# Optimization experiments

Measured on AMD Instinct MI355X. Metric: run time of the kernel, lower is better.

The kernel has to match this reference:

```python
import jax, jax.numpy as jnp
from jax import lax
import numpy as np

GAMMA = 0.5
LENS = 0.3
B_J0 = 0.1
# eval-mode BN with running_mean=0, running_var=1, weight=0.1, bias=0 -> pure scale
BN_SCALE = 0.1 / np.sqrt(1.0 + 1e-5)


def _gaussian(x, mu, sigma):
    return jnp.exp(-(x - mu) ** 2 / (2.0 * sigma ** 2)) / np.sqrt(2.0 * np.pi) / sigma


@jax.custom_vjp
def act_fun_adp(x):
    return (x > 0).astype(x.dtype)


def _act_fwd(x):
    return act_fun_adp(x), x


def _act_bwd(x, g):
    scale, hight = 6.0, 0.15
    temp = (_gaussian(x, 0.0, LENS) * (1.0 + hight)
            - _gaussian(x, LENS, scale * LENS) * hight
            - _gaussian(x, -LENS, scale * LENS) * hight)
    return (g * temp * GAMMA,)


act_fun_adp.defvjp(_act_fwd, _act_bwd)


def _lin(x, w, b):
    return x @ w.T + b


def _mem_update_adp(inp, mem, spk, tau_adp, tau_m, b):
    b = tau_adp * b + (1.0 - tau_adp) * spk
    B = B_J0 + 1.8 * b
    mem = mem + (-mem + inp) * tau_m
    spk = act_fun_adp(mem - B)
    mem = (1.0 - spk) * mem
    return mem, spk, b


def _snn(inputs, h, p):
    (w1x, b1x, w1r, b1r, w1m, b1m, w1a, b1a,
     w2x, b2x, w2r, b2r, w2m, b2m, w2a, b2a,
     w3x, b3x, w3m, b3m) = p

    def step(h, x):
        mem1, spk1, bb1, mem2, spk2, bb2, mem3 = h
        dense1 = BN_SCALE * _lin(x, w1x, b1x) + BN_SCALE * _lin(spk1, w1r, b1r)
        tauM1 = jax.nn.sigmoid(_lin(jnp.concatenate([dense1, mem1], -1), w1m, b1m))
        tauA1 = jax.nn.sigmoid(_lin(jnp.concatenate([dense1, bb1], -1), w1a, b1a))
        nmem1, nspk1, nbb1 = _mem_update_adp(dense1, mem1, spk1, tauA1, tauM1, bb1)
        # dropout in eval mode = identity; layer2_r uses PREVIOUS spk1 (h[1]) as in source
        dense2 = BN_SCALE * _lin(nspk1, w2x, b2x) + BN_SCALE * _lin(spk1, w2r, b2r)
        tauM2 = jax.nn.sigmoid(_lin(jnp.concatenate([dense2, mem2], -1), w2m, b2m))
        tauA2 = jax.nn.sigmoid(_lin(jnp.concatenate([dense2, bb2], -1), w2a, b2a))
        nmem2, nspk2, nbb2 = _mem_update_adp(dense2, mem2, spk2, tauA2, tauM2, bb2)
        dense3 = BN_SCALE * _lin(nspk2, w3x, b3x)
        tauM3 = jax.nn.sigmoid(_lin(jnp.concatenate([dense3, mem3], -1), w3m, b3m))
        nmem3 = (1.0 - tauM3) * mem3 + dense3 * tauM3
        out = jax.nn.log_softmax(nmem3, axis=1)
        return (nmem1, nspk1, nbb1, nmem2, nspk2, nbb2, nmem3), out

    xs = jnp.swapaxes(inputs, 0, 1)  # [T, B, Din]
    hT, outs = lax.scan(step, h, xs)
    return outs, hT  # outs: [T, B, O]


def setup_inputs() -> dict:
    key = jax.random.key(0)
    B, T, DIN, H, O = 128, 100, 700, 1024, 20
    ks = jax.random.split(key, 16)
    d = {
        'inputs': jax.random.normal(ks[0], (B, T, DIN), jnp.float32),
        'h0': jnp.zeros((B, H)), 'h1': jnp.zeros((B, H)), 'h2': jnp.zeros((B, H)),
        'h3': jnp.zeros((B, H)), 'h4': jnp.zeros((B, H)), 'h5': jnp.zeros((B, H)),
        'h6': jnp.zeros((B, O)),
        'w1x': jax.random.normal(ks[1], (H, DIN)) * 0.03,
        'b1x': jnp.zeros((H,)),
        'w1r': jax.random.normal(ks[2], (H, H)) * 0.03,
        'b1r': jnp.zeros((H,)),
        'w1m': jax.random.normal(ks[3], (H, 2 * H)) * 0.02,
        'b1m': jnp.zeros((H,)),
        'w1a': jax.random.normal(ks[4], (H, 2 * H)) * 0.02,
        'b1a': jnp.zeros((H,)),
        'w2x': jax.random.normal(ks[5], (H, H)) * 0.03,
        'b2x': jnp.zeros((H,)),
        'w2r': jax.random.normal(ks[6], (H, H)) * 0.03,
        'b2r': jnp.zeros((H,)),
        'w2m': jax.random.normal(ks[7], (H, 2 * H)) * 0.02,
        'b2m': jnp.zeros((H,)),
        'w2a': jax.random.normal(ks[8], (H, 2 * H)) * 0.02,
        'b2a': jnp.zeros((H,)),
        'w3x': jax.random.normal(ks[9], (O, H)) * 0.03,
        'b3x': jnp.zeros((O,)),
        'w3m': jax.random.normal(ks[10], (O, 2 * O)) * 0.02,
        'b3m': jnp.zeros((O,)),
    }
    return d


def reference(inputs, h0, h1, h2, h3, h4, h5, h6,
              w1x, b1x, w1r, b1r, w1m, b1m, w1a, b1a,
              w2x, b2x, w2r, b2r, w2m, b2m, w2a, b2a,
              w3x, b3x, w3m, b3m):
    h = (h0, h1, h2, h3, h4, h5, h6)
    p = (w1x, b1x, w1r, b1r, w1m, b1m, w1a, b1a,
         w2x, b2x, w2r, b2r, w2m, b2m, w2a, b2a,
         w3x, b3x, w3m, b3m)
    outs, hT = _snn(inputs, h, p)
    return (outs,) + hT
```

## Files before the change

kernel.cpp:

```cpp
#include <hip/hip_runtime.h>
#include <cmath>


namespace {

constexpr int BB = 128, TT = 100, DIN = 700, HH = 1024, OO = 20;
constexpr int BH = BB * HH;
constexpr int XP = 704;
constexpr float SBN = 0.09999950000374996f;

typedef __attribute__((ext_vector_type(8))) __bf16 bf16x8;
typedef __attribute__((ext_vector_type(4))) float f32x4;

__device__ __forceinline__ float sigm(float x) { return 1.f / (1.f + expf(-x)); }

__device__ __forceinline__ unsigned short f2bf(float x) {
  union { float f; unsigned u; } a; a.f = x;
  unsigned u = a.u; u += 0x7fffu + ((u >> 16) & 1u);
  return (unsigned short)(u >> 16);
}
__device__ __forceinline__ float bf2f(unsigned short h) {
  union { unsigned u; float f; } a; a.u = ((unsigned)h) << 16; return a.f;
}


struct MSeg {
  const unsigned short* Ah; const unsigned short* Al;
  const unsigned short* Wh; const unsigned short* Wl;
  float* P;
  int ldk, KS, nsplit, nblkn, mbs, ldp;
  size_t planesz;
};
struct MArgs { MSeg s[8]; int bstart[9]; int nseg; };

__global__ __launch_bounds__(256)
void mfma_seg(MArgs ma) {
  int bid = blockIdx.x, si = 0;
  while (si + 1 < ma.nseg && bid >= ma.bstart[si + 1]) si++;
  MSeg sg = ma.s[si]; bid -= ma.bstart[si];
  const int per_m = sg.nblkn * sg.nsplit;
  const int mb = bid / per_m;
  const int rr = bid - mb * per_m;
  const int nb = rr / sg.nsplit, sp = rr - nb * sg.nsplit;
  const int n0 = nb * 64;
  const int m0 = mb * 128;
  const int kbeg = sp * sg.KS, kend = kbeg + sg.KS;
  const int lane = threadIdx.x & 63, wave = threadIdx.x >> 6;
  const int wm = (wave >> 1) * 64, wn = (wave & 1) * 32;
  const int quad = lane >> 4, r16 = lane & 15;
  const int ldk = sg.ldk;
  const int nkb = ldk >> 5;
  const bool three = (sg.Al != nullptr);
  const unsigned short* ah = sg.Ah + (size_t)(m0 + wm + r16) * ldk + quad * 8;
  const unsigned short* al = three ? sg.Al + (size_t)(m0 + wm + r16) * ldk + quad * 8 : ah;
  const size_t tb = (size_t)((n0 + wn) >> 4) * nkb * 512 + (size_t)lane * 8;
  const unsigned short* wh = sg.Wh + tb;
  const unsigned short* wl = sg.Wl + tb;

  f32x4 acc[4][2];
#pragma unroll
  for (int i = 0; i < 4; i++)
#pragma unroll
    for (int j = 0; j < 2; j++) acc[i][j] = (f32x4){0.f, 0.f, 0.f, 0.f};

  auto loadf = [&](int k, bf16x8* Ab, bf16x8* ALb, bf16x8* Bb, bf16x8* BLb) {
    const int kb = k >> 5;
#pragma unroll
    for (int mt = 0; mt < 4; mt++)
      Ab[mt] = *(const bf16x8*)(ah + (size_t)mt * 16 * ldk + k);
#pragma unroll
    for (int nt = 0; nt < 2; nt++) {
      Bb[nt] = *(const bf16x8*)(wh + ((size_t)nt * nkb + kb) * 512);
      BLb[nt] = *(const bf16x8*)(wl + ((size_t)nt * nkb + kb) * 512);
    }
    if (three) {
#pragma unroll
      for (int mt = 0; mt < 4; mt++)
        ALb[mt] = *(const bf16x8*)(al + (size_t)mt * 16 * ldk + k);
    }
  };
  auto domfma = [&](bf16x8* Ab, bf16x8* ALb, bf16x8* Bb, bf16x8* BLb) {
#pragma unroll
    for (int mt = 0; mt < 4; mt++)
#pragma unroll
      for (int nt = 0; nt < 2; nt++) {
        acc[mt][nt] = __builtin_amdgcn_mfma_f32_16x16x32_bf16(Ab[mt], Bb[nt], acc[mt][nt], 0, 0, 0);
        acc[mt][nt] = __builtin_amdgcn_mfma_f32_16x16x32_bf16(Ab[mt], BLb[nt], acc[mt][nt], 0, 0, 0);
        if (three)
          acc[mt][nt] = __builtin_amdgcn_mfma_f32_16x16x32_bf16(ALb[mt], Bb[nt], acc[mt][nt], 0, 0, 0);
      }
  };

  bf16x8 A0[4], L0[4], B0[2], C0[2];
  bf16x8 A1[4], L1[4], B1[2], C1[2];
  int k = kbeg;
  loadf(k, A0, L0, B0, C0);
  while (true) {
    int k1 = k + 32;
    bool more1 = k1 < kend;
    if (more1) loadf(k1, A1, L1, B1, C1);
    domfma(A0, L0, B0, C0);
    if (!more1) break;
    int k2 = k1 + 32;
    bool more2 = k2 < kend;
    if (more2) loadf(k2, A0, L0, B0, C0);
    domfma(A1, L1, B1, C1);
    if (!more2) break;
    k = k2;
  }

  const int outl = n0 >> 10;
  const int col0 = (n0 & 1023) + wn;
  float* P = sg.P + (size_t)(outl * sg.nsplit + sp) * sg.planesz;
#pragma unroll
  for (int mt = 0; mt < 4; mt++)
#pragma unroll
    for (int nt = 0; nt < 2; nt++)
#pragma unroll
      for (int r = 0; r < 4; r++)
        P[(size_t)(m0 + wm + mt * 16 + quad * 4 + r) * sg.ldp + col0 + nt * 16 + r16] = acc[mt][nt][r];
}

struct CJob { const float* src; int ldsrc, rows, cols, rrows, mode; unsigned short* dh; unsigned short* dl; int lddst; float scale; };
struct CArgs { CJob j[16]; int bstart[17]; int njob; };

__global__ __launch_bounds__(256)
void cvt_pack(CArgs ca) {
  int bid = blockIdx.x, ji = 0;
  while (ji + 1 < ca.njob && bid >= ca.bstart[ji + 1]) ji++;
  CJob j = ca.j[ji]; bid -= ca.bstart[ji];
  size_t total = (size_t)j.rows * j.lddst;
  size_t base = ((size_t)bid * 256 + threadIdx.x) * 4;
  const int nkb = j.lddst >> 5;
#pragma unroll
  for (int e = 0; e < 4; e++) {
    size_t i = base + e;
    if (i >= total) break;
    int r, c;
    if (j.mode == 2) {
      r = (int)(i / j.lddst); c = (int)(i - (size_t)r * j.lddst);
    } else {
      size_t tile = i >> 9;
      int within = (int)(i & 511);
      int lane = within >> 3, jj = within & 7;
      int r16 = lane & 15, quad = lane >> 4;
      int ntile = (int)(tile / nkb), kb = (int)(tile - (size_t)ntile * nkb);
      r = ntile * 16 + r16;
      c = kb * 32 + quad * 8 + jj;
    }
    float v = 0.f;
    if (c < j.cols && r < j.rrows)
      v = j.scale * (j.mode == 1 ? j.src[(size_t)c * j.ldsrc + r]
                                 : j.src[(size_t)r * j.ldsrc + c]);
    unsigned short hh = f2bf(v);
    j.dh[i] = hh;
    j.dl[i] = f2bf(v - bf2f(hh));
  }
}

__global__ __launch_bounds__(256)
void init_state(const float* h0, const float* h1, const float* h2, const float* h3,
                const float* h4, const float* h5, const float* h6, const float* inputs,
                float* mem1, float* spk1, float* bb1, float* mem2, float* spk2, float* bb2,
                float* mem3, unsigned short* spk1bf,
                unsigned short* m1h, unsigned short* m1l, unsigned short* b1h, unsigned short* b1l,
                unsigned short* m2h, unsigned short* m2l, unsigned short* b2h, unsigned short* b2l,
                unsigned short* xh0, unsigned short* xl0) {
  int idx = blockIdx.x * 256 + threadIdx.x;
  if (idx < BH) {
    float v;
    v = h0[idx]; mem1[idx] = v; { unsigned short h = f2bf(v); m1h[idx] = h; m1l[idx] = f2bf(v - bf2f(h)); }
    v = h1[idx]; spk1[idx] = v; spk1bf[idx] = f2bf(v);
    v = h2[idx]; bb1[idx] = v;  { unsigned short h = f2bf(v); b1h[idx] = h; b1l[idx] = f2bf(v - bf2f(h)); }
    v = h3[idx]; mem2[idx] = v; { unsigned short h = f2bf(v); m2h[idx] = h; m2l[idx] = f2bf(v - bf2f(h)); }
    spk2[idx] = h4[idx];
    v = h5[idx]; bb2[idx] = v;  { unsigned short h = f2bf(v); b2h[idx] = h; b2l[idx] = f2bf(v - bf2f(h)); }
  }
  if (idx < BB * OO) mem3[idx] = h6[idx];
  if (idx < BB * XP) {
    int b = idx / XP, c = idx - b * XP;
    float v = (c < DIN) ? inputs[(size_t)b * TT * DIN + c] : 0.f;
    unsigned short hh = f2bf(v);
    xh0[idx] = hh; xl0[idx] = f2bf(v - bf2f(hh));
  }
}

__global__ __launch_bounds__(256)
void ew1m(const float* Pbuf, const float* b1x, const float* b1r,
          const float* cb1m, const float* cb1a,
          float* mem1, float* spk1, float* bb1, unsigned short* spk1bf,
          unsigned short* m1h, unsigned short* m1l, unsigned short* b1h_, unsigned short* b1l_) {
  int idx = blockIdx.x * 256 + threadIdx.x;
  int n = idx & (HH - 1);
  constexpr int D1S[6]   = {0, 1, 6, 7, 8, 9};
  constexpr int T1MS[10] = {2, 3, 10, 11, 12, 13, 30, 31, 32, 33};
  constexpr int T1AS[10] = {4, 5, 14, 15, 16, 17, 34, 35, 36, 37};
  float d1 = SBN * (b1x[n] + b1r[n]);
#pragma unroll
  for (int i = 0; i < 6; i++) d1 += Pbuf[(size_t)D1S[i] * BH + idx];
  float pm = cb1m[n];
#pragma unroll
  for (int i = 0; i < 10; i++) pm += Pbuf[(size_t)T1MS[i] * BH + idx];
  float pa = cb1a[n];
#pragma unroll
  for (int i = 0; i < 10; i++) pa += Pbuf[(size_t)T1AS[i] * BH + idx];
  float tM = sigm(pm), tA = sigm(pa);
  float spo = spk1[idx], bo = bb1[idx], mo = mem1[idx];
  float nb = tA * bo + (1.f - tA) * spo;
  float Bth = 0.1f + 1.8f * nb;
  float nm = mo + (d1 - mo) * tM;
  float sp = (nm - Bth) > 0.f ? 1.f : 0.f;
  nm = (1.f - sp) * nm;
  mem1[idx] = nm; spk1[idx] = sp; bb1[idx] = nb;
  spk1bf[idx] = f2bf(sp);
  { unsigned short h = f2bf(nm); m1h[idx] = h; m1l[idx] = f2bf(nm - bf2f(h)); }
  { unsigned short h = f2bf(nb); b1h_[idx] = h; b1l_[idx] = f2bf(nb - bf2f(h)); }
}

__global__ __launch_bounds__(1024)
void ew2l3m(const float* Pbuf, const float* b2x, const float* b2r,
            const float* cb2m, const float* cb2a,
            float* mem2, float* spk2, float* bb2, float* mem3,
            unsigned short* m2h, unsigned short* m2l, unsigned short* b2h_, unsigned short* b2l_,
            const float* w3x, const float* b3x, const float* w3m, const float* b3m,
            float* outs, const float* inputs, unsigned short* xh_next, unsigned short* xl_next,
            int t) {
  int b = blockIdx.x;
  int n = threadIdx.x;
  size_t idx = (size_t)b * HH + n;
  constexpr int D2S[8]   = {18, 19, 20, 21, 46, 47, 48, 49};
  constexpr int T2MS[12] = {22, 23, 24, 25, 38, 39, 40, 41, 50, 51, 52, 53};
  constexpr int T2AS[12] = {26, 27, 28, 29, 42, 43, 44, 45, 54, 55, 56, 57};
  float d2 = SBN * (b2x[n] + b2r[n]);
#pragma unroll
  for (int i = 0; i < 8; i++) d2 += Pbuf[(size_t)D2S[i] * BH + idx];
  float pm = cb2m[n];
#pragma unroll
  for (int i = 0; i < 12; i++) pm += Pbuf[(size_t)T2MS[i] * BH + idx];
  float pa = cb2a[n];
#pragma unroll
  for (int i = 0; i < 12; i++) pa += Pbuf[(size_t)T2AS[i] * BH + idx];
  float tM = sigm(pm), tA = sigm(pa);
  float spo = spk2[idx], bo = bb2[idx], mo = mem2[idx];
  float nb = tA * bo + (1.f - tA) * spo;
  float Bth = 0.1f + 1.8f * nb;
  float nm = mo + (d2 - mo) * tM;
  float sp = (nm - Bth) > 0.f ? 1.f : 0.f;
  nm = (1.f - sp) * nm;
  mem2[idx] = nm; spk2[idx] = sp; bb2[idx] = nb;
  { unsigned short h = f2bf(nm); m2h[idx] = h; m2l[idx] = f2bf(nm - bf2f(h)); }
  { unsigned short h = f2bf(nb); b2h_[idx] = h; b2l_[idx] = f2bf(nb - bf2f(h)); }

  if (t + 1 < TT && n < XP) {
    float v = (n < DIN) ? inputs[((size_t)b * TT + (t + 1)) * DIN + n] : 0.f;
    unsigned short hh = f2bf(v);
    xh_next[b * XP + n] = hh;
    xl_next[b * XP + n] = f2bf(v - bf2f(hh));
  }

  __shared__ float smsp[HH];
  __shared__ float d3s[OO];
  __shared__ float nm3s[OO];
  smsp[n] = sp;
  __syncthreads();

  int wv = n >> 6, ln = n & 63;
  for (int o = wv; o < OO; o += 16) {
    float s = 0.f;
    for (int j = ln; j < HH; j += 64) s += smsp[j] * w3x[(size_t)o * HH + j];
    for (int off = 32; off > 0; off >>= 1) s += __shfl_down(s, off, 64);
    if (ln == 0) d3s[o] = SBN * (s + b3x[o]);
  }
  __syncthreads();

  if (n < OO) {
    float acc = b3m[n];
#pragma unroll
    for (int k = 0; k < OO; k++) acc += d3s[k] * w3m[n * 40 + k];
#pragma unroll
    for (int k = 0; k < OO; k++) acc += mem3[b * OO + k] * w3m[n * 40 + 20 + k];
    float tau = sigm(acc);
    nm3s[n] = (1.f - tau) * mem3[b * OO + n] + d3s[n] * tau;
  }
  __syncthreads();

  if (n < OO) {
    float mx = -1e30f;
#pragma unroll
    for (int k = 0; k < OO; k++) mx = fmaxf(mx, nm3s[k]);
    float se = 0.f;
#pragma unroll
    for (int k = 0; k < OO; k++) se += expf(nm3s[k] - mx);
    float lse = mx + logf(se);
    outs[((size_t)t * BB + b) * OO + n] = nm3s[n] - lse;
    mem3[b * OO + n] = nm3s[n];
  }
}


struct Seg {
  const float* A; const float* W; float* P;
  int lda, ldw, ldp, K, KS, nsplit, mblks, nblks, nbound, xmap, xoff;
  float scale;
};
constexpr int MAXSEG = 13;
struct SegArgs { Seg s[MAXSEG]; int bstart[MAXSEG + 1]; int nseg; };

__global__ __launch_bounds__(256)
void seg_gemm(SegArgs sa) {
  int bid = blockIdx.x;
  int si = 0;
  while (si + 1 < sa.nseg && bid >= sa.bstart[si + 1]) si++;
  const Seg sg = sa.s[si];
  bid -= sa.bstart[si];
  const int per_m = sg.nblks * sg.nsplit;
  const int mb = bid / per_m;
  const int rr = bid - mb * per_m;
  const int nb = rr / sg.nsplit;
  const int sp = rr - nb * sg.nsplit;
  const int m0 = mb * 128, n0 = nb * 32;
  const int kbeg = sp * sg.KS;
  const int kend = min(sg.K, kbeg + sg.KS);

  __shared__ float As[32][132];
  __shared__ float Ws[32][36];

  const int t = threadIdx.x;
  const int cg = t & 7;
  const int rg = t >> 3;

  float acc[4][4];
#pragma unroll
  for (int i = 0; i < 4; i++)
#pragma unroll
    for (int j = 0; j < 4; j++) acc[i][j] = 0.f;

  for (int k0 = kbeg; k0 < kend; k0 += 32) {
#pragma unroll
    for (int i = 0; i < 4; i++) {
      int fl = t + i * 256;
      int row = fl >> 3, kq = fl & 7;
      int kg = k0 + kq * 4;
      float4 v = make_float4(0.f, 0.f, 0.f, 0.f);
      if (kg < kend) {
        const float* src = sg.xmap
            ? sg.A + ((size_t)(m0 + row) * TT + sg.xoff) * DIN + kg
            : sg.A + (size_t)(m0 + row) * sg.lda + kg;
        v = *(const float4*)src;
      }
      As[kq * 4 + 0][row] = v.x;
      As[kq * 4 + 1][row] = v.y;
      As[kq * 4 + 2][row] = v.z;
      As[kq * 4 + 3][row] = v.w;
    }
    {
      int n = t >> 3, kq = t & 7;
      int kg = k0 + kq * 4;
      float4 v = make_float4(0.f, 0.f, 0.f, 0.f);
      if (kg < kend && (n0 + n) < sg.nbound)
        v = *(const float4*)(sg.W + (size_t)(n0 + n) * sg.ldw + kg);
      Ws[kq * 4 + 0][n] = v.x;
      Ws[kq * 4 + 1][n] = v.y;
      Ws[kq * 4 + 2][n] = v.z;
      Ws[kq * 4 + 3][n] = v.w;
    }
    __syncthreads();
#pragma unroll
    for (int kk = 0; kk < 32; kk++) {
      float4 av = *(const float4*)&As[kk][rg * 4];
      float4 wv = *(const float4*)&Ws[kk][cg * 4];
      acc[0][0] += av.x * wv.x; acc[0][1] += av.x * wv.y; acc[0][2] += av.x * wv.z; acc[0][3] += av.x * wv.w;
      acc[1][0] += av.y * wv.x; acc[1][1] += av.y * wv.y; acc[1][2] += av.y * wv.z; acc[1][3] += av.y * wv.w;
      acc[2][0] += av.z * wv.x; acc[2][1] += av.z * wv.y; acc[2][2] += av.z * wv.z; acc[2][3] += av.z * wv.w;
      acc[3][0] += av.w * wv.x; acc[3][1] += av.w * wv.y; acc[3][2] += av.w * wv.z; acc[3][3] += av.w * wv.w;
    }
    __syncthreads();
  }
  float* P = sg.P + ((size_t)sp * sg.mblks * 128 + m0) * sg.ldp;
#pragma unroll
  for (int i = 0; i < 4; i++) {
    float4 v = make_float4(sg.scale * acc[i][0], sg.scale * acc[i][1],
                           sg.scale * acc[i][2], sg.scale * acc[i][3]);
    *(float4*)&P[(size_t)(rg * 4 + i) * sg.ldp + n0 + cg * 4] = v;
  }
}

struct TJob { const float* src; float* dst; int rows, cols, ntc; };
struct TArgs { TJob j[4]; int tstart[5]; };

__global__ __launch_bounds__(256)
void transpose4(TArgs ta) {
  int bid = blockIdx.x;
  int ji = 0;
  while (ji + 1 < 4 && bid >= ta.tstart[ji + 1]) ji++;
  TJob j = ta.j[ji];
  bid -= ta.tstart[ji];
  int tr = bid / j.ntc, tc = bid - tr * j.ntc;
  int r0 = tr * 32, c0 = tc * 32;
  __shared__ float tile[32][33];
  int tx = threadIdx.x & 31, ty = threadIdx.x >> 5;
#pragma unroll
  for (int p = 0; p < 4; p++) {
    int r = r0 + ty + p * 8, c = c0 + tx;
    if (r < j.rows && c < j.cols) tile[ty + p * 8][tx] = j.src[(size_t)r * j.cols + c];
  }
  __syncthreads();
#pragma unroll
  for (int p = 0; p < 4; p++) {
    int c = c0 + ty + p * 8, r = r0 + tx;
    if (c < j.cols && r < j.rows) j.dst[(size_t)c * j.rows + r] = tile[tx][ty + p * 8];
// ... 408 lines not shown
  float* mem1 = ws + off; off += BH;
  float* spk1 = ws + off; off += BH;
  float* bb1  = ws + off; off += BH;
  float* mem2 = ws + off; off += BH;
  float* spk2 = ws + off; off += BH;
  float* bb2  = ws + off; off += BH;
  float* mem3 = ws + off; off += BB * OO;
  float* cb1m = ws + off; off += HH;
  float* cb1a = ws + off; off += HH;
  float* cb2m = ws + off; off += HH;
  float* cb2a = ws + off; off += HH;
  float* w1rT = ws + off; off += (size_t)HH * HH;
  float* w2rT = ws + off; off += (size_t)HH * HH;
  float* w2xT = ws + off; off += (size_t)HH * HH;
  float* w1xT = ws + off; off += (size_t)DIN * HH;
  float* G1mT  = ws + off; off += (size_t)HH * HH;
  float* G1aT  = ws + off; off += (size_t)HH * HH;
  float* H1MT  = ws + off; off += (size_t)HH * 704;
  float* H1AT  = ws + off; off += (size_t)HH * 704;
  float* G2rmT = ws + off; off += (size_t)HH * HH;
  float* G2raT = ws + off; off += (size_t)HH * HH;
  float* G2xmT = ws + off; off += (size_t)HH * HH;
  float* G2xaT = ws + off; off += (size_t)HH * HH;
  float* Pbuf  = ws + off; off += (size_t)32 * BH;
  if (ws_size < off * sizeof(float)) {
    launch_tier3(d_in, d_out, d_ws, ws_size, stream);
    return;
  }

  hipMemcpyAsync(mem1, h[0], (size_t)BH * 4, hipMemcpyDeviceToDevice, stream);
  hipMemcpyAsync(spk1, h[1], (size_t)BH * 4, hipMemcpyDeviceToDevice, stream);
  hipMemcpyAsync(bb1,  h[2], (size_t)BH * 4, hipMemcpyDeviceToDevice, stream);
  hipMemcpyAsync(mem2, h[3], (size_t)BH * 4, hipMemcpyDeviceToDevice, stream);
  hipMemcpyAsync(spk2, h[4], (size_t)BH * 4, hipMemcpyDeviceToDevice, stream);
  hipMemcpyAsync(bb2,  h[5], (size_t)BH * 4, hipMemcpyDeviceToDevice, stream);
  hipMemcpyAsync(mem3, h[6], (size_t)BB * OO * 4, hipMemcpyDeviceToDevice, stream);

  {
    TArgs ta{};
    ta.j[0] = TJob{w1r, w1rT, HH, HH, 32};
    ta.j[1] = TJob{w2r, w2rT, HH, HH, 32};
    ta.j[2] = TJob{w2x, w2xT, HH, HH, 32};
    ta.j[3] = TJob{w1x, w1xT, HH, DIN, 22};
    ta.tstart[0] = 0; ta.tstart[1] = 1024; ta.tstart[2] = 2048;
    ta.tstart[3] = 3072; ta.tstart[4] = 3072 + 32 * 22;
    transpose4<<<ta.tstart[4], 256, 0, stream>>>(ta);
  }
  bias_prep<<<1024, 256, 0, stream>>>(b1x, b1r, b2x, b2r, w1m, b1m, w1a, b1a,
                                      w2m, b2m, w2a, b2a, cb1m, cb1a, cb2m, cb2a);
  {
    SegArgs sa{};
    int nb = 0, c = 0;
    auto add = [&](const float* A, int lda, const float* W, int ldw, int nbound,
                   float* P, int ldp, int nblks) {
      sa.s[c] = Seg{A, W, P, lda, ldw, ldp, HH, HH, 1, 8, nblks, nbound, 0, 0, 1.0f};
      sa.bstart[c] = nb; nb += 8 * nblks; c++;
    };
    add(w1m, 2048, w1rT, 1024, 1024, G1mT, 1024, 32);
    add(w1a, 2048, w1rT, 1024, 1024, G1aT, 1024, 32);
    add(w1m, 2048, w1xT, 1024, DIN, H1MT, 704, 22);
    add(w1a, 2048, w1xT, 1024, DIN, H1AT, 704, 22);
    add(w2m, 2048, w2rT, 1024, 1024, G2rmT, 1024, 32);
    add(w2a, 2048, w2rT, 1024, 1024, G2raT, 1024, 32);
    add(w2m, 2048, w2xT, 1024, 1024, G2xmT, 1024, 32);
    add(w2a, 2048, w2xT, 1024, 1024, G2xaT, 1024, 32);
    sa.bstart[c] = nb; sa.nseg = c;
    seg_gemm<<<nb, 256, 0, stream>>>(sa);
  }

  for (int t = 0; t < TT; ++t) {
    {
      SegArgs sa{};
      int nb = 0, c = 0;
      auto add = [&](const float* A, int lda, int xmap, const float* W, int ldw,
                     int K, int KS, int slot, float scale) {
        sa.s[c] = Seg{A, W, Pbuf + (size_t)slot * BH, lda, ldw, 1024, K, KS, 2, 1, 32,
                      1024, xmap, t, scale};
        sa.bstart[c] = nb; nb += 64; c++;
      };
      add(inputs, 0, 1, w1x, DIN, DIN, 352, 0, SBN);
      add(spk1, 1024, 0, w1r, 1024, 1024, 512, 2, SBN);
      add(inputs, 0, 1, H1MT, 704, DIN, 352, 4, SBN);
      add(spk1, 1024, 0, G1mT, 1024, 1024, 512, 6, SBN);
      add(mem1, 1024, 0, w1m + 1024, 2048, 1024, 512, 8, 1.0f);
      add(inputs, 0, 1, H1AT, 704, DIN, 352, 10, SBN);
      add(spk1, 1024, 0, G1aT, 1024, 1024, 512, 12, SBN);
      add(bb1, 1024, 0, w1a + 1024, 2048, 1024, 512, 14, 1.0f);
      add(spk1, 1024, 0, w2r, 1024, 1024, 512, 16, SBN);
      add(spk1, 1024, 0, G2rmT, 1024, 1024, 512, 18, SBN);
      add(mem2, 1024, 0, w2m + 1024, 2048, 1024, 512, 20, 1.0f);
      add(spk1, 1024, 0, G2raT, 1024, 1024, 512, 22, SBN);
      add(bb2, 1024, 0, w2a + 1024, 2048, 1024, 512, 24, 1.0f);
      sa.bstart[c] = nb; sa.nseg = c;
      seg_gemm<<<nb, 256, 0, stream>>>(sa);
    }
    ew1<<<BH / 256, 256, 0, stream>>>(Pbuf, b1x, b1r, cb1m, cb1a, mem1, spk1, bb1);
    {
      SegArgs sa{};
      int nb = 0, c = 0;
      auto add = [&](const float* W, int slot) {
        sa.s[c] = Seg{spk1, W, Pbuf + (size_t)slot * BH, 1024, 1024, 1024, 1024, 512,
                      2, 1, 32, 1024, 0, 0, SBN};
        sa.bstart[c] = nb; nb += 64; c++;
      };
      add(w2x, 26);
      add(G2xmT, 28);
      add(G2xaT, 30);
      sa.bstart[c] = nb; sa.nseg = c;
      seg_gemm<<<nb, 256, 0, stream>>>(sa);
    }
    ew2_layer3<<<BB, 1024, 0, stream>>>(Pbuf, b2x, b2r, cb2m, cb2a, mem2, spk2, bb2,
                                        mem3, w3x, b3x, w3m, b3m, (float*)d_out, t);
  }

  float* out = (float*)d_out;
  size_t o = (size_t)TT * BB * OO;
  hipMemcpyAsync(out + o, mem1, (size_t)BH * 4, hipMemcpyDeviceToDevice, stream); o += BH;
  hipMemcpyAsync(out + o, spk1, (size_t)BH * 4, hipMemcpyDeviceToDevice, stream); o += BH;
  hipMemcpyAsync(out + o, bb1,  (size_t)BH * 4, hipMemcpyDeviceToDevice, stream); o += BH;
  hipMemcpyAsync(out + o, mem2, (size_t)BH * 4, hipMemcpyDeviceToDevice, stream); o += BH;
  hipMemcpyAsync(out + o, spk2, (size_t)BH * 4, hipMemcpyDeviceToDevice, stream); o += BH;
  hipMemcpyAsync(out + o, bb2,  (size_t)BH * 4, hipMemcpyDeviceToDevice, stream); o += BH;
  hipMemcpyAsync(out + o, mem3, (size_t)BB * OO * 4, hipMemcpyDeviceToDevice, stream);
}

}

extern "C" void kernel_launch(void* const* d_in, const int* in_sizes, int n_in,
                              void* d_out, int out_size, void* d_ws, size_t ws_size,
                              hipStream_t stream) {
  const float* inputs = (const float*)d_in[0];
  const float* h0 = (const float*)d_in[1]; const float* h1 = (const float*)d_in[2];
  const float* h2 = (const float*)d_in[3]; const float* h3 = (const float*)d_in[4];
  const float* h4 = (const float*)d_in[5]; const float* h5 = (const float*)d_in[6];
  const float* h6 = (const float*)d_in[7];
  const float* w1x = (const float*)d_in[8];  const float* b1x = (const float*)d_in[9];
  const float* w1r = (const float*)d_in[10]; const float* b1r = (const float*)d_in[11];
  const float* w1m = (const float*)d_in[12]; const float* b1m = (const float*)d_in[13];
  const float* w1a = (const float*)d_in[14]; const float* b1a = (const float*)d_in[15];
  const float* w2x = (const float*)d_in[16]; const float* b2x = (const float*)d_in[17];
  const float* w2r = (const float*)d_in[18]; const float* b2r = (const float*)d_in[19];
  const float* w2m = (const float*)d_in[20]; const float* b2m = (const float*)d_in[21];
  const float* w2a = (const float*)d_in[22]; const float* b2a = (const float*)d_in[23];
  const float* w3x = (const float*)d_in[24]; const float* b3x = (const float*)d_in[25];
  const float* w3m = (const float*)d_in[26]; const float* b3m = (const float*)d_in[27];

  char* base = (char*)d_ws;
  size_t cur = 0;
  auto alloc = [&](size_t bytes) -> char* {
    char* p = base + cur;
    cur += (bytes + 255) & ~(size_t)255;
    return p;
  };
  float* mem1 = (float*)alloc((size_t)BH * 4);
  float* spk1 = (float*)alloc((size_t)BH * 4);
  float* bb1  = (float*)alloc((size_t)BH * 4);
  float* mem2 = (float*)alloc((size_t)BH * 4);
  float* spk2 = (float*)alloc((size_t)BH * 4);
  float* bb2  = (float*)alloc((size_t)BH * 4);
  float* mem3 = (float*)alloc((size_t)BB * OO * 4);
  float* cb1m = (float*)alloc(HH * 4);
  float* cb1a = (float*)alloc(HH * 4);
  float* cb2m = (float*)alloc(HH * 4);
  float* cb2a = (float*)alloc(HH * 4);
  unsigned short* spk1bf = (unsigned short*)alloc((size_t)BH * 2);
  unsigned short* m1h = (unsigned short*)alloc((size_t)BH * 2);
  unsigned short* m1l = (unsigned short*)alloc((size_t)BH * 2);
  unsigned short* b1h = (unsigned short*)alloc((size_t)BH * 2);
  unsigned short* b1l = (unsigned short*)alloc((size_t)BH * 2);
  unsigned short* m2h = (unsigned short*)alloc((size_t)BH * 2);
  unsigned short* m2l = (unsigned short*)alloc((size_t)BH * 2);
  unsigned short* b2h = (unsigned short*)alloc((size_t)BH * 2);
  unsigned short* b2l = (unsigned short*)alloc((size_t)BH * 2);
  unsigned short* xh[2]; unsigned short* xl[2];
  xh[0] = (unsigned short*)alloc((size_t)BB * XP * 2);
  xl[0] = (unsigned short*)alloc((size_t)BB * XP * 2);
  xh[1] = (unsigned short*)alloc((size_t)BB * XP * 2);
  xl[1] = (unsigned short*)alloc((size_t)BB * XP * 2);
  unsigned short* XWh  = (unsigned short*)alloc((size_t)3 * HH * XP * 2);
  unsigned short* XWl  = (unsigned short*)alloc((size_t)3 * HH * XP * 2);
  unsigned short* WSPKh = (unsigned short*)alloc((size_t)6 * HH * HH * 2);
  unsigned short* WSPKl = (unsigned short*)alloc((size_t)6 * HH * HH * 2);
  unsigned short* WM1h = (unsigned short*)alloc((size_t)HH * HH * 2);
  unsigned short* WM1l = (unsigned short*)alloc((size_t)HH * HH * 2);
  unsigned short* WB1h = (unsigned short*)alloc((size_t)HH * HH * 2);
  unsigned short* WB1l = (unsigned short*)alloc((size_t)HH * HH * 2);
  unsigned short* WM2h = (unsigned short*)alloc((size_t)HH * HH * 2);
  unsigned short* WM2l = (unsigned short*)alloc((size_t)HH * HH * 2);
  unsigned short* WB2h = (unsigned short*)alloc((size_t)HH * HH * 2);
  unsigned short* WB2l = (unsigned short*)alloc((size_t)HH * HH * 2);
  unsigned short* WSBh = (unsigned short*)alloc((size_t)3 * HH * HH * 2);
  unsigned short* WSBl = (unsigned short*)alloc((size_t)3 * HH * HH * 2);
  size_t scratch_fl = (size_t)6 * HH * HH + (size_t)2 * HH * XP;
  size_t pbuf_fl = (size_t)58 * BH;
  size_t shared_fl = scratch_fl > pbuf_fl ? scratch_fl : pbuf_fl;
  char* shared = alloc(shared_fl * 4);

  if (ws_size < cur) {
    launch_tier2(d_in, d_out, d_ws, ws_size, stream);
    return;
  }

  float* G1m  = (float*)shared;
  float* G1a  = G1m + (size_t)HH * HH;
  float* G2rm = G1a + (size_t)HH * HH;
  float* G2ra = G2rm + (size_t)HH * HH;
  float* G2xm = G2ra + (size_t)HH * HH;
  float* G2xa = G2xm + (size_t)HH * HH;
  float* H1M  = G2xa + (size_t)HH * HH;
  float* H1A  = H1M + (size_t)HH * XP;
  float* Pbuf = (float*)shared;

  unsigned short* opW1rTh = WSPKh;
  unsigned short* opW1rTl = WSPKh + (size_t)1 * HH * HH;
  unsigned short* opW2rTh = WSPKh + (size_t)2 * HH * HH;
  unsigned short* opW2rTl = WSPKh + (size_t)3 * HH * HH;
  unsigned short* opW2xTh = WSPKh + (size_t)4 * HH * HH;
  unsigned short* opW2xTl = WSPKh + (size_t)5 * HH * HH;
  unsigned short* opW1xTh = WSPKl;
  unsigned short* opW1xTl = WSPKl + (size_t)XP * HH;
  unsigned short* opW1mh  = WSPKl + (size_t)2 * XP * HH;
  unsigned short* opW1ml  = opW1mh + (size_t)HH * HH;
  unsigned short* opW1ah  = opW1ml + (size_t)HH * HH;
  unsigned short* opW1al  = opW1ah + (size_t)HH * HH;
  unsigned short* opW2mh  = WM1h;
  unsigned short* opW2ml  = WM1l;
  unsigned short* opW2ah  = WB1h;
  unsigned short* opW2al  = WB1l;

  init_state<<<BH / 256, 256, 0, stream>>>(h0, h1, h2, h3, h4, h5, h6, inputs,
      mem1, spk1, bb1, mem2, spk2, bb2, mem3, spk1bf,
      m1h, m1l, b1h, b1l, m2h, m2l, b2h, b2l, xh[0], xl[0]);

  bias_prep<<<1024, 256, 0, stream>>>(b1x, b1r, b2x, b2r, w1m, b1m, w1a, b1a,
                                      w2m, b2m, w2a, b2a, cb1m, cb1a, cb2m, cb2a);

  {
    CArgs ca{};
    int nb = 0, c = 0;
    auto add = [&](const float* src, int ldsrc, int rows, int cols, int rrows, int mode,
                   unsigned short* dh, unsigned short* dl, int lddst, float scale) {
      ca.j[c] = CJob{src, ldsrc, rows, cols, rrows, mode, dh, dl, lddst, scale};
      ca.bstart[c] = nb;
      nb += (int)(((size_t)rows * lddst + 1023) / 1024);
      c++;
    };
    add(w1r, HH, HH, HH, HH, 1, opW1rTh, opW1rTl, HH, SBN);
    add(w2r, HH, HH, HH, HH, 1, opW2rTh, opW2rTl, HH, SBN);
    add(w2x, HH, HH, HH, HH, 1, opW2xTh, opW2xTl, HH, SBN);
    add(w1x, DIN, XP, HH, DIN, 1, opW1xTh, opW1xTl, HH, SBN);
    add(w1m, 2048, HH, HH, HH, 2, opW1mh, opW1ml, HH, 1.f);
    add(w1a, 2048, HH, HH, HH, 2, opW1ah, opW1al, HH, 1.f);
    add(w2m, 2048, HH, HH, HH, 2, opW2mh, opW2ml, HH, 1.f);
    add(w2a, 2048, HH, HH, HH, 2, opW2ah, opW2al, HH, 1.f);
    ca.bstart[c] = nb; ca.njob = c;
    cvt_pack<<<nb, 256, 0, stream>>>(ca);
  }

  {
    MArgs ma{};
    int nb = 0, c = 0;
    auto add = [&](const unsigned short* Ah, const unsigned short* Al,
                   const unsigned short* Wh, const unsigned short* Wl,
                   float* P, int nblkn, int ldp) {
      ma.s[c] = MSeg{Ah, Al, Wh, Wl, P, HH, HH, 1, nblkn, 8, ldp, (size_t)HH * HH};
      ma.bstart[c] = nb; nb += 8 * nblkn; c++;
    };
    add(opW1mh, opW1ml, opW1rTh, opW1rTl, G1m, 16, HH);
    add(opW1ah, opW1al, opW1rTh, opW1rTl, G1a, 16, HH);
    add(opW2mh, opW2ml, opW2rTh, opW2rTl, G2rm, 16, HH);
    add(opW2ah, opW2al, opW2rTh, opW2rTl, G2ra, 16, HH);
    add(opW2mh, opW2ml, opW2xTh, opW2xTl, G2xm, 16, HH);
    add(opW2ah, opW2al, opW2xTh, opW2xTl, G2xa, 16, HH);
    add(opW1mh, opW1ml, opW1xTh, opW1xTl, H1M, 11, XP);
    add(opW1ah, opW1al, opW1xTh, opW1xTl, H1A, 11, XP);
    ma.bstart[c] = nb; ma.nseg = c;
    mfma_seg<<<nb, 256, 0, stream>>>(ma);
  }

  {
    CArgs ca{};
    int nb = 0, c = 0;
    auto add = [&](const float* src, int ldsrc, int rows, int cols,
                   unsigned short* dh, unsigned short* dl, int lddst, float scale) {
      ca.j[c] = CJob{src, ldsrc, rows, cols, rows, 0, dh, dl, lddst, scale};
      ca.bstart[c] = nb;
      nb += (int)(((size_t)rows * lddst + 1023) / 1024);
      c++;
    };
    add(w1x, DIN, HH, DIN, XWh, XWl, XP, SBN);
    add(H1M, XP, HH, XP, XWh + (size_t)HH * XP, XWl + (size_t)HH * XP, XP, 1.f);
    add(H1A, XP, HH, XP, XWh + (size_t)2 * HH * XP, XWl + (size_t)2 * HH * XP, XP, 1.f);
    add(w1r, HH, HH, HH, WSPKh, WSPKl, HH, SBN);
    add(G1m, HH, HH, HH, WSPKh + (size_t)HH * HH, WSPKl + (size_t)HH * HH, HH, 1.f);
    add(G1a, HH, HH, HH, WSPKh + (size_t)2 * HH * HH, WSPKl + (size_t)2 * HH * HH, HH, 1.f);
    add(w2r, HH, HH, HH, WSPKh + (size_t)3 * HH * HH, WSPKl + (size_t)3 * HH * HH, HH, SBN);
    add(G2rm, HH, HH, HH, WSPKh + (size_t)4 * HH * HH, WSPKl + (size_t)4 * HH * HH, HH, 1.f);
    add(G2ra, HH, HH, HH, WSPKh + (size_t)5 * HH * HH, WSPKl + (size_t)5 * HH * HH, HH, 1.f);
    add(w1m + 1024, 2048, HH, HH, WM1h, WM1l, HH, 1.f);
    add(w1a + 1024, 2048, HH, HH, WB1h, WB1l, HH, 1.f);
    add(w2m + 1024, 2048, HH, HH, WM2h, WM2l, HH, 1.f);
    add(w2a + 1024, 2048, HH, HH, WB2h, WB2l, HH, 1.f);
    add(w2x, HH, HH, HH, WSBh, WSBl, HH, SBN);
    add(G2xm, HH, HH, HH, WSBh + (size_t)HH * HH, WSBl + (size_t)HH * HH, HH, 1.f);
    add(G2xa, HH, HH, HH, WSBh + (size_t)2 * HH * HH, WSBl + (size_t)2 * HH * HH, HH, 1.f);
    ca.bstart[c] = nb; ca.njob = c;
    cvt_pack<<<nb, 256, 0, stream>>>(ca);
  }

  for (int t = 0; t < TT; ++t) {
    {
      MArgs ma{};
      int nb = 0, c = 0;
      auto add = [&](const unsigned short* Ah, const unsigned short* Al,
                     const unsigned short* Wh, const unsigned short* Wl,
                     int ldk, int KS, int nsplit, int nblkn, int baseslot) {
        ma.s[c] = MSeg{Ah, Al, Wh, Wl, Pbuf + (size_t)baseslot * BH, ldk, KS, nsplit,
                       nblkn, 1, 1024, (size_t)BH};
        ma.bstart[c] = nb; nb += nblkn * nsplit; c++;
      };
      add(xh[t & 1], xl[t & 1], XWh, XWl, XP, 352, 2, 48, 0);
      add(spk1bf, nullptr, WSPKh, WSPKl, HH, 256, 4, 96, 6);
      add(m1h, m1l, WM1h, WM1l, HH, 256, 4, 16, 30);
      add(b1h, b1l, WB1h, WB1l, HH, 256, 4, 16, 34);
      add(m2h, m2l, WM2h, WM2l, HH, 256, 4, 16, 38);
      add(b2h, b2l, WB2h, WB2l, HH, 256, 4, 16, 42);
      ma.bstart[c] = nb; ma.nseg = c;
      mfma_seg<<<nb, 256, 0, stream>>>(ma);
    }
    ew1m<<<BH / 256, 256, 0, stream>>>(Pbuf, b1x, b1r, cb1m, cb1a,
                                       mem1, spk1, bb1, spk1bf, m1h, m1l, b1h, b1l);
    {
      MArgs ma{};
      ma.s[0] = MSeg{spk1bf, nullptr, WSBh, WSBl, Pbuf + (size_t)46 * BH, HH, 256, 4,
                     48, 1, 1024, (size_t)BH};
      ma.bstart[0] = 0; ma.bstart[1] = 192; ma.nseg = 1;
      mfma_seg<<<192, 256, 0, stream>>>(ma);
    }
    ew2l3m<<<BB, 1024, 0, stream>>>(Pbuf, b2x, b2r, cb2m, cb2a,
                                    mem2, spk2, bb2, mem3, m2h, m2l, b2h, b2l,
                                    w3x, b3x, w3m, b3m, (float*)d_out,
                                    inputs, xh[(t + 1) & 1], xl[(t + 1) & 1], t);
  }

  float* out = (float*)d_out;
  size_t o = (size_t)TT * BB * OO;
  hipMemcpyAsync(out + o, mem1, (size_t)BH * 4, hipMemcpyDeviceToDevice, stream); o += BH;
  hipMemcpyAsync(out + o, spk1, (size_t)BH * 4, hipMemcpyDeviceToDevice, stream); o += BH;
  hipMemcpyAsync(out + o, bb1,  (size_t)BH * 4, hipMemcpyDeviceToDevice, stream); o += BH;
  hipMemcpyAsync(out + o, mem2, (size_t)BH * 4, hipMemcpyDeviceToDevice, stream); o += BH;
  hipMemcpyAsync(out + o, spk2, (size_t)BH * 4, hipMemcpyDeviceToDevice, stream); o += BH;
  hipMemcpyAsync(out + o, bb2,  (size_t)BH * 4, hipMemcpyDeviceToDevice, stream); o += BH;
  hipMemcpyAsync(out + o, mem3, (size_t)BB * OO * 4, hipMemcpyDeviceToDevice, stream);
}
```

Baseline: 6.173 ms.

## Hoist input projections for all timesteps into one batched GEMM

The input-dependent matmuls (x through the w1x, tauM and tauA projections), which do not depend on recurrent state, are now computed once before the time loop as a single large GEMM over all 100 timesteps. The input is converted to split-bf16 in one pass, and the per-step elementwise kernel reads the precomputed slices. This removes the x segment from each step's serial GEMM launch and gives one well-occupied GEMM in its place. It needs a large extra workspace (3*T*B*H floats), and it falls back to the old path when the workspace is too small.

```diff
diff --git a/kernel.cpp b/kernel.cpp
--- a/kernel.cpp
+++ b/kernel.cpp
@@ -159,6 +159,22 @@
 }
 
 __global__ __launch_bounds__(256)
+void cvt_x_all(const float* inputs, unsigned short* xh, unsigned short* xl) {
+  size_t base = ((size_t)blockIdx.x * 256 + threadIdx.x) * 4;
+  size_t total = (size_t)TT * BB * XP;
+#pragma unroll
+  for (int e = 0; e < 4; e++) {
+    size_t i = base + e;
+    if (i >= total) break;
+    int m = (int)(i / XP), c = (int)(i - (size_t)m * XP);
+    int t = m / BB, b = m - t * BB;
+    float v = (c < DIN) ? inputs[((size_t)b * TT + t) * DIN + c] : 0.f;
+    unsigned short hh = f2bf(v);
+    xh[i] = hh; xl[i] = f2bf(v - bf2f(hh));
+  }
+}
+
+__global__ __launch_bounds__(256)
 void init_state(const float* h0, const float* h1, const float* h2, const float* h3,
                 const float* h4, const float* h5, const float* h6, const float* inputs,
                 float* mem1, float* spk1, float* bb1, float* mem2, float* spk2, float* bb2,
@@ -177,7 +193,7 @@
     v = h5[idx]; bb2[idx] = v;  { unsigned short h = f2bf(v); b2h[idx] = h; b2l[idx] = f2bf(v - bf2f(h)); }
   }
   if (idx < BB * OO) mem3[idx] = h6[idx];
-  if (idx < BB * XP) {
+  if (xh0 != nullptr && idx < BB * XP) {
     int b = idx / XP, c = idx - b * XP;
     float v = (c < DIN) ? inputs[(size_t)b * TT * DIN + c] : 0.f;
     unsigned short hh = f2bf(v);
@@ -185,25 +201,41 @@
   }
 }
 
+template<int HOISTX>
 __global__ __launch_bounds__(256)
-void ew1m(const float* Pbuf, const float* b1x, const float* b1r,
-          const float* cb1m, const float* cb1a,
+void ew1m(const float* Pbuf, const float* Ud1, const float* UtM, const float* UtA,
+          const float* b1x, const float* b1r, const float* cb1m, const float* cb1a,
           float* mem1, float* spk1, float* bb1, unsigned short* spk1bf,
-          unsigned short* m1h, unsigned short* m1l, unsigned short* b1h_, unsigned short* b1l_) {
+          unsigned short* m1h, unsigned short* m1l, unsigned short* b1h_, unsigned short* b1l_,
+          int t) {
   int idx = blockIdx.x * 256 + threadIdx.x;
   int n = idx & (HH - 1);
-  constexpr int D1S[6]   = {0, 1, 6, 7, 8, 9};
-  constexpr int T1MS[10] = {2, 3, 10, 11, 12, 13, 30, 31, 32, 33};
-  constexpr int T1AS[10] = {4, 5, 14, 15, 16, 17, 34, 35, 36, 37};
   float d1 = SBN * (b1x[n] + b1r[n]);
-#pragma unroll
-  for (int i = 0; i < 6; i++) d1 += Pbuf[(size_t)D1S[i] * BH + idx];
-  float pm = cb1m[n];
-#pragma unroll
-  for (int i = 0; i < 10; i++) pm += Pbuf[(size_t)T1MS[i] * BH + idx];
-  float pa = cb1a[n];
-#pragma unroll
-  for (int i = 0; i < 10; i++) pa += Pbuf[(size_t)T1AS[i] * BH + idx];
+  float pm = cb1m[n], pa = cb1a[n];
+  if (HOISTX) {
+    size_t uo = (size_t)t * BH + idx;
+    d1 += Ud1[uo]; pm += UtM[uo]; pa += UtA[uo];
+#pragma unroll
+    for (int i = 0; i < 4; i++) d1 += Pbuf[(size_t)(0 + i) * BH + idx];
+#pragma unroll
+    for (int i = 0; i < 4; i++) pm += Pbuf[(size_t)(4 + i) * BH + idx];
+#pragma unroll
+    for (int i = 0; i < 4; i++) pm += Pbuf[(size_t)(24 + i) * BH + idx];
+#pragma unroll
+    for (int i = 0; i < 4; i++) pa += Pbuf[(size_t)(8 + i) * BH + idx];
+#pragma unroll
+    for (int i = 0; i < 4; i++) pa += Pbuf[(size_t)(28 + i) * BH + idx];
+  } else {
+    constexpr int D1S[6]   = {0, 1, 6, 7, 8, 9};
+    constexpr int T1MS[10] = {2, 3, 10, 11, 12, 13, 30, 31, 32, 33};
+    constexpr int T1AS[10] = {4, 5, 14, 15, 16, 17, 34, 35, 36, 37};
+#pragma unroll
+    for (int i = 0; i < 6; i++) d1 += Pbuf[(size_t)D1S[i] * BH + idx];
+#pragma unroll
+    for (int i = 0; i < 10; i++) pm += Pbuf[(size_t)T1MS[i] * BH + idx];
+#pragma unroll
+    for (int i = 0; i < 10; i++) pa += Pbuf[(size_t)T1AS[i] * BH + idx];
+  }
   float tM = sigm(pm), tA = sigm(pa);
   float spo = spk1[idx], bo = bb1[idx], mo = mem1[idx];
   float nb = tA * bo + (1.f - tA) * spo;
@@ -217,6 +249,7 @@
   { unsigned short h = f2bf(nb); b1h_[idx] = h; b1l_[idx] = f2bf(nb - bf2f(h)); }
 }
 
+template<int HOISTX>
 __global__ __launch_bounds__(1024)
 void ew2l3m(const float* Pbuf, const float* b2x, const float* b2r,
             const float* cb2m, const float* cb2a,
@@ -228,18 +261,36 @@
   int b = blockIdx.x;
   int n = threadIdx.x;
   size_t idx = (size_t)b * HH + n;
-  constexpr int D2S[8]   = {18, 19, 20, 21, 46, 47, 48, 49};
-  constexpr int T2MS[12] = {22, 23, 24, 25, 38, 39, 40, 41, 50, 51, 52, 53};
-  constexpr int T2AS[12] = {26, 27, 28, 29, 42, 43, 44, 45, 54, 55, 56, 57};
   float d2 = SBN * (b2x[n] + b2r[n]);
-#pragma unroll
-  for (int i = 0; i < 8; i++) d2 += Pbuf[(size_t)D2S[i] * BH + idx];
-  float pm = cb2m[n];
-#pragma unroll
-  for (int i = 0; i < 12; i++) pm += Pbuf[(size_t)T2MS[i] * BH + idx];
-  float pa = cb2a[n];
-#pragma unroll
-  for (int i = 0; i < 12; i++) pa += Pbuf[(size_t)T2AS[i] * BH + idx];
+  float pm = cb2m[n], pa = cb2a[n];
+  if (HOISTX) {
+#pragma unroll
+    for (int i = 0; i < 4; i++) d2 += Pbuf[(size_t)(12 + i) * BH + idx];
+#pragma unroll
+    for (int i = 0; i < 4; i++) d2 += Pbuf[(size_t)(40 + i) * BH + idx];
+#pragma unroll
+    for (int i = 0; i < 4; i++) pm += Pbuf[(size_t)(16 + i) * BH + idx];
+#pragma unroll
+    for (int i = 0; i < 4; i++) pm += Pbuf[(size_t)(32 + i) * BH + idx];
+#pragma unroll
+    for (int i = 0; i < 4; i++) pm += Pbuf[(size_t)(44 + i) * BH + idx];
+#pragma unroll
+    for (int i = 0; i < 4; i++) pa += Pbuf[(size_t)(20 + i) * BH + idx];
+#pragma unroll
+    for (int i = 0; i < 4; i++) pa += Pbuf[(size_t)(36 + i) * BH + idx];
+#pragma unroll
+    for (int i = 0; i < 4; i++) pa += Pbuf[(size_t)(48 + i) * BH + idx];
+  } else {
+    constexpr int D2S[8]   = {18, 19, 20, 21, 46, 47, 48, 49};
+    constexpr int T2MS[12] = {22, 23, 24, 25, 38, 39, 40, 41, 50, 51, 52, 53};
+    constexpr int T2AS[12] = {26, 27, 28, 29, 42, 43, 44, 45, 54, 55, 56, 57};
+#pragma unroll
+    for (int i = 0; i < 8; i++) d2 += Pbuf[(size_t)D2S[i] * BH + idx];
+#pragma unroll
+    for (int i = 0; i < 12; i++) pm += Pbuf[(size_t)T2MS[i] * BH + idx];
+#pragma unroll
+    for (int i = 0; i < 12; i++) pa += Pbuf[(size_t)T2AS[i] * BH + idx];
+  }
   float tM = sigm(pm), tA = sigm(pa);
   float spo = spk2[idx], bo = bb2[idx], mo = mem2[idx];
   float nb = tA * bo + (1.f - tA) * spo;
@@ -251,11 +302,13 @@
   { unsigned short h = f2bf(nm); m2h[idx] = h; m2l[idx] = f2bf(nm - bf2f(h)); }
   { unsigned short h = f2bf(nb); b2h_[idx] = h; b2l_[idx] = f2bf(nb - bf2f(h)); }
 
-  if (t + 1 < TT && n < XP) {
-    float v = (n < DIN) ? inputs[((size_t)b * TT + (t + 1)) * DIN + n] : 0.f;
-    unsigned short hh = f2bf(v);
-    xh_next[b * XP + n] = hh;
-    xl_next[b * XP + n] = f2bf(v - bf2f(hh));
+  if (!HOISTX) {
+    if (t + 1 < TT && n < XP) {
+      float v = (n < DIN) ? inputs[((size_t)b * TT + (t + 1)) * DIN + n] : 0.f;
+      unsigned short hh = f2bf(v);
+      xh_next[b * XP + n] = hh;
+      xl_next[b * XP + n] = f2bf(v - bf2f(hh));
+    }
   }
 
   __shared__ float smsp[HH];
@@ -970,53 +1023,76 @@
     cur += (bytes + 255) & ~(size_t)255;
     return p;
   };
-  float* mem1 = (float*)alloc((size_t)BH * 4);
-  float* spk1 = (float*)alloc((size_t)BH * 4);
-  float* bb1  = (float*)alloc((size_t)BH * 4);
-  float* mem2 = (float*)alloc((size_t)BH * 4);
-  float* spk2 = (float*)alloc((size_t)BH * 4);
-  float* bb2  = (float*)alloc((size_t)BH * 4);
-  float* mem3 = (float*)alloc((size_t)BB * OO * 4);
-  float* cb1m = (float*)alloc(HH * 4);
-  float* cb1a = (float*)alloc(HH * 4);
-  float* cb2m = (float*)alloc(HH * 4);
-  float* cb2a = (float*)alloc(HH * 4);
-  unsigned short* spk1bf = (unsigned short*)alloc((size_t)BH * 2);
-  unsigned short* m1h = (unsigned short*)alloc((size_t)BH * 2);
-  unsigned short* m1l = (unsigned short*)alloc((size_t)BH * 2);
-  unsigned short* b1h = (unsigned short*)alloc((size_t)BH * 2);
-  unsigned short* b1l = (unsigned short*)alloc((size_t)BH * 2);
-  unsigned short* m2h = (unsigned short*)alloc((size_t)BH * 2);
-  unsigned short* m2l = (unsigned short*)alloc((size_t)BH * 2);
-  unsigned short* b2h = (unsigned short*)alloc((size_t)BH * 2);
-  unsigned short* b2l = (unsigned short*)alloc((size_t)BH * 2);
-  unsigned short* xh[2]; unsigned short* xl[2];
-  xh[0] = (unsigned short*)alloc((size_t)BB * XP * 2);
-  xl[0] = (unsigned short*)alloc((size_t)BB * XP * 2);
-  xh[1] = (unsigned short*)alloc((size_t)BB * XP * 2);
-  xl[1] = (unsigned short*)alloc((size_t)BB * XP * 2);
-  unsigned short* XWh  = (unsigned short*)alloc((size_t)3 * HH * XP * 2);
-  unsigned short* XWl  = (unsigned short*)alloc((size_t)3 * HH * XP * 2);
-  unsigned short* WSPKh = (unsigned short*)alloc((size_t)6 * HH * HH * 2);
-  unsigned short* WSPKl = (unsigned short*)alloc((size_t)6 * HH * HH * 2);
-  unsigned short* WM1h = (unsigned short*)alloc((size_t)HH * HH * 2);
-  unsigned short* WM1l = (unsigned short*)alloc((size_t)HH * HH * 2);
-  unsigned short* WB1h = (unsigned short*)alloc((size_t)HH * HH * 2);
-  unsigned short* WB1l = (unsigned short*)alloc((size_t)HH * HH * 2);
-  unsigned short* WM2h = (unsigned short*)alloc((size_t)HH * HH * 2);
-  unsigned short* WM2l = (unsigned short*)alloc((size_t)HH * HH * 2);
-  unsigned short* WB2h = (unsigned short*)alloc((size_t)HH * HH * 2);
-  unsigned short* WB2l = (unsigned short*)alloc((size_t)HH * HH * 2);
-  unsigned short* WSBh = (unsigned short*)alloc((size_t)3 * HH * HH * 2);
-  unsigned short* WSBl = (unsigned short*)alloc((size_t)3 * HH * HH * 2);
-  size_t scratch_fl = (size_t)6 * HH * HH + (size_t)2 * HH * XP;
-  size_t pbuf_fl = (size_t)58 * BH;
-  size_t shared_fl = scratch_fl > pbuf_fl ? scratch_fl : pbuf_fl;
-  char* shared = alloc(shared_fl * 4);
-
-  if (ws_size < cur) {
-    launch_tier2(d_in, d_out, d_ws, ws_size, stream);
-    return;
+
+  float *mem1, *spk1, *bb1, *mem2, *spk2, *bb2, *mem3;
+  float *cb1m, *cb1a, *cb2m, *cb2a;
+  unsigned short *spk1bf, *m1h, *m1l, *b1h, *b1l, *m2h, *m2l, *b2h, *b2l;
+  unsigned short *xh[2], *xl[2];
+  unsigned short *XWh, *XWl, *WSPKh, *WSPKl, *WM1h, *WM1l, *WB1h, *WB1l;
+  unsigned short *WM2h, *WM2l, *WB2h, *WB2l, *WSBh, *WSBl;
+  unsigned short *xbigh = nullptr, *xbigl = nullptr;
+  float* U1x = nullptr;
+  char* shared = nullptr;
+
+  auto doLayout = [&](bool hx) -> size_t {
+    cur = 0;
+    mem1 = (float*)alloc((size_t)BH * 4);
+    spk1 = (float*)alloc((size_t)BH * 4);
+    bb1  = (float*)alloc((size_t)BH * 4);
+    mem2 = (float*)alloc((size_t)BH * 4);
+    spk2 = (float*)alloc((size_t)BH * 4);
+    bb2  = (float*)alloc((size_t)BH * 4);
+    mem3 = (float*)alloc((size_t)BB * OO * 4);
+    cb1m = (float*)alloc(HH * 4);
+    cb1a = (float*)alloc(HH * 4);
+    cb2m = (float*)alloc(HH * 4);
+    cb2a = (float*)alloc(HH * 4);
+    spk1bf = (unsigned short*)alloc((size_t)BH * 2);
+    m1h = (unsigned short*)alloc((size_t)BH * 2);
+    m1l = (unsigned short*)alloc((size_t)BH * 2);
+    b1h = (unsigned short*)alloc((size_t)BH * 2);
+    b1l = (unsigned short*)alloc((size_t)BH * 2);
+    m2h = (unsigned short*)alloc((size_t)BH * 2);
+    m2l = (unsigned short*)alloc((size_t)BH * 2);
+    b2h = (unsigned short*)alloc((size_t)BH * 2);
+    b2l = (unsigned short*)alloc((size_t)BH * 2);
+    xh[0] = (unsigned short*)alloc((size_t)BB * XP * 2);
+    xl[0] = (unsigned short*)alloc((size_t)BB * XP * 2);
+    xh[1] = (unsigned short*)alloc((size_t)BB * XP * 2);
+    xl[1] = (unsigned short*)alloc((size_t)BB * XP * 2);
+    XWh  = (unsigned short*)alloc((size_t)3 * HH * XP * 2);
+    XWl  = (unsigned short*)alloc((size_t)3 * HH * XP * 2);
+    WSPKh = (unsigned short*)alloc((size_t)6 * HH * HH * 2);
+    WSPKl = (unsigned short*)alloc((size_t)6 * HH * HH * 2);
+    WM1h = (unsigned short*)alloc((size_t)HH * HH * 2);
+    WM1l = (unsigned short*)alloc((size_t)HH * HH * 2);
+    WB1h = (unsigned short*)alloc((size_t)HH * HH * 2);
+    WB1l = (unsigned short*)alloc((size_t)HH * HH * 2);
+    WM2h = (unsigned short*)alloc((size_t)HH * HH * 2);
+    WM2l = (unsigned short*)alloc((size_t)HH * HH * 2);
+    WB2h = (unsigned short*)alloc((size_t)HH * HH * 2);
+    WB2l = (unsigned short*)alloc((size_t)HH * HH * 2);
+    WSBh = (unsigned short*)alloc((size_t)3 * HH * HH * 2);
+    WSBl = (unsigned short*)alloc((size_t)3 * HH * HH * 2);
+    if (hx) {
+      xbigh = (unsigned short*)alloc((size_t)TT * BB * XP * 2);
+      xbigl = (unsigned short*)alloc((size_t)TT * BB * XP * 2);
+      U1x   = (float*)alloc((size_t)3 * TT * BH * 4);
+    } else {
+      xbigh = xbigl = nullptr; U1x = nullptr;
+    }
+    size_t scratch_fl = (size_t)6 * HH * HH + (size_t)2 * HH * XP;
+    shared = alloc(scratch_fl * 4);
+    return cur;
+  };
+
+  bool hoistx = true;
+  if (doLayout(true) > ws_size) {
+    hoistx = false;
+    if (doLayout(false) > ws_size) {
+      launch_tier2(d_in, d_out, d_ws, ws_size, stream);
+      return;
+    }
   }
 
   float* G1m  = (float*)shared;
@@ -1028,6 +1104,9 @@
   float* H1M  = G2xa + (size_t)HH * HH;
   float* H1A  = H1M + (size_t)HH * XP;
   float* Pbuf = (float*)shared;
+  float* Ud1 = U1x;
+  float* UtM = hoistx ? U1x + (size_t)TT * BH : nullptr;
+  float* UtA = hoistx ? U1x + (size_t)2 * TT * BH : nullptr;
 
   unsigned short* opW1rTh = WSPKh;
   unsigned short* opW1rTl = WSPKh + (size_t)1 * HH * HH;
@@ -1048,7 +1127,12 @@
 
   init_state<<<BH / 256, 256, 0, stream>>>(h0, h1, h2, h3, h4, h5, h6, inputs,
       mem1, spk1, bb1, mem2, spk2, bb2, mem3, spk1bf,
-      m1h, m1l, b1h, b1l, m2h, m2l, b2h, b2l, xh[0], xl[0]);
+      m1h, m1l, b1h, b1l, m2h, m2l, b2h, b2l,
+      hoistx ? nullptr : xh[0], hoistx ? nullptr : xl[0]);
+  if (hoistx) {
+    int nblk = (int)(((size_t)TT * BB * XP / 4 + 255) / 256);
+    cvt_x_all<<<nblk, 256, 0, stream>>>(inputs, xbigh, xbigl);
+  }
 
   bias_prep<<<1024, 256, 0, stream>>>(b1x, b1r, b2x, b2r, w1m, b1m, w1a, b1a,
                                       w2m, b2m, w2a, b2a, cb1m, cb1a, cb2m, cb2a);
@@ -1126,8 +1210,33 @@
     cvt_pack<<<nb, 256, 0, stream>>>(ca);
   }
 
+  if (hoistx) {
+    MArgs ma{};
+    ma.s[0] = MSeg{xbigh, xbigl, XWh, XWl, U1x, XP, XP, 1, 48, 100, 1024,
+                   (size_t)TT * BH};
+    ma.bstart[0] = 0; ma.bstart[1] = 100 * 48; ma.nseg = 1;
+    mfma_seg<<<100 * 48, 256, 0, stream>>>(ma);
+  }
+
   for (int t = 0; t < TT; ++t) {
-    {
+    if (hoistx) {
+      MArgs ma{};
+      int nb = 0, c = 0;
+      auto add = [&](const unsigned short* Ah, const unsigned short* Al,
+                     const unsigned short* Wh, const unsigned short* Wl,
+                     int nblkn, int baseslot) {
+        ma.s[c] = MSeg{Ah, Al, Wh, Wl, Pbuf + (size_t)baseslot * BH, HH, 256, 4,
+                       nblkn, 1, 1024, (size_t)BH};
+        ma.bstart[c] = nb; nb += nblkn * 4; c++;
+      };
+      add(spk1bf, nullptr, WSPKh, WSPKl, 96, 0);
+      add(m1h, m1l, WM1h, WM1l, 16, 24);
+      add(b1h, b1l, WB1h, WB1l, 16, 28);
+      add(m2h, m2l, WM2h, WM2l, 16, 32);
+      add(b2h, b2l, WB2h, WB2l, 16, 36);
+      ma.bstart[c] = nb; ma.nseg = c;
+      mfma_seg<<<nb, 256, 0, stream>>>(ma);
+    } else {
       MArgs ma{};
       int nb = 0, c = 0;
       auto add = [&](const unsigned short* Ah, const unsigned short* Al,
@@ -1146,19 +1255,31 @@
       ma.bstart[c] = nb; ma.nseg = c;
       mfma_seg<<<nb, 256, 0, stream>>>(ma);
     }
-    ew1m<<<BH / 256, 256, 0, stream>>>(Pbuf, b1x, b1r, cb1m, cb1a,
-                                       mem1, spk1, bb1, spk1bf, m1h, m1l, b1h, b1l);
+    if (hoistx)
+      ew1m<1><<<BH / 256, 256, 0, stream>>>(Pbuf, Ud1, UtM, UtA, b1x, b1r, cb1m, cb1a,
+                                            mem1, spk1, bb1, spk1bf, m1h, m1l, b1h, b1l, t);
+    else
+      ew1m<0><<<BH / 256, 256, 0, stream>>>(Pbuf, nullptr, nullptr, nullptr, b1x, b1r,
+                                            cb1m, cb1a, mem1, spk1, bb1, spk1bf,
+                                            m1h, m1l, b1h, b1l, t);
     {
       MArgs ma{};
-      ma.s[0] = MSeg{spk1bf, nullptr, WSBh, WSBl, Pbuf + (size_t)46 * BH, HH, 256, 4,
+      int baseslot = hoistx ? 40 : 46;
+      ma.s[0] = MSeg{spk1bf, nullptr, WSBh, WSBl, Pbuf + (size_t)baseslot * BH, HH, 256, 4,
                      48, 1, 1024, (size_t)BH};
       ma.bstart[0] = 0; ma.bstart[1] = 192; ma.nseg = 1;
       mfma_seg<<<192, 256, 0, stream>>>(ma);
     }
-    ew2l3m<<<BB, 1024, 0, stream>>>(Pbuf, b2x, b2r, cb2m, cb2a,
-                                    mem2, spk2, bb2, mem3, m2h, m2l, b2h, b2l,
-                                    w3x, b3x, w3m, b3m, (float*)d_out,
-                                    inputs, xh[(t + 1) & 1], xl[(t + 1) & 1], t);
+    if (hoistx)
+      ew2l3m<1><<<BB, 1024, 0, stream>>>(Pbuf, b2x, b2r, cb2m, cb2a,
+                                         mem2, spk2, bb2, mem3, m2h, m2l, b2h, b2l,
+                                         w3x, b3x, w3m, b3m, (float*)d_out,
+                                         inputs, nullptr, nullptr, t);
+    else
+      ew2l3m<0><<<BB, 1024, 0, stream>>>(Pbuf, b2x, b2r, cb2m, cb2a,
+                                         mem2, spk2, bb2, mem3, m2h, m2l, b2h, b2l,
+                                         w3x, b3x, w3m, b3m, (float*)d_out,
+                                         inputs, xh[(t + 1) & 1], xl[(t + 1) & 1], t);
   }
 
   float* out = (float*)d_out;
```

Result: no change. 6.185 ms (+0.2%).
